# Performance work log

Measured on AMD Instinct MI355X. Metric: run time of the kernel, lower is better.

Reference implementation:

```python
import jax, jax.numpy as jnp
import numpy as np

B, C, N, K = 2, 64, 16384, 16
C_OUT = 64


def setup_inputs() -> dict:
    key = jax.random.key(0)
    k1, k2, k3, k4 = jax.random.split(key, 4)
    x = jax.random.normal(k1, (B, C, N), dtype=jnp.float32)
    edge_index = jax.random.randint(k2, (2, B, N, K), 0, N, dtype=jnp.int64)
    # 1x1 Conv2d params: weight [C_out, 3C], bias [C_out]
    W = jax.random.normal(k3, (C_OUT, 3 * C), dtype=jnp.float32) * (1.0 / np.sqrt(3 * C))
    b = jax.random.normal(k4, (C_OUT,), dtype=jnp.float32) * 0.01
    return {"x": x, "edge_index": edge_index, "W": W, "b": b}


def _gather_nodes(x, idx):
    # x: [B, C, N], idx: [B, N, K] -> [B, C, N, K]
    return jax.vmap(lambda xb, ib: xb[:, ib])(x, idx)


def reference(x, edge_index, W, b):
    # x: [B, C, N]; edge_index: [2, B, N, K]
    x_i = _gather_nodes(x, edge_index[1])          # center features  [B,C,N,K]
    x_j = _gather_nodes(x, edge_index[0])          # neighbor features [B,C,N,K]
    edge_features = x_j - x_i                      # [B,C,N,K]
    global_feature = jnp.mean(x, axis=2, keepdims=True)  # [B,C,1] global mean over nodes
    global_rep = jnp.broadcast_to(global_feature[..., None], x_i.shape)  # [B,C,N,K]
    combined = jnp.concatenate([x_i, edge_features, global_rep], axis=1)  # [B,3C,N,K]
    # BasicConv: 1x1 conv + ReLU (norm=None)
    out = jnp.einsum("bcnk,oc->bonk", combined, W) + b[None, :, None, None]
    out = jax.nn.relu(out)
    return jnp.max(out, axis=-1, keepdims=True)    # [B,C_out,N,1]
```

## Files before the change

### kernel.cpp

```cpp
#include <hip/hip_runtime.h>


#define NNODES 16384
#define NCH 64

typedef _Float16 half8 __attribute__((ext_vector_type(8)));
typedef float f32x2 __attribute__((ext_vector_type(2)));
typedef float f32x4 __attribute__((ext_vector_type(4)));

__global__ __launch_bounds__(64) void prep_kernel(const float* __restrict__ W,
                                                  float2* __restrict__ ABg,
                                                  float* __restrict__ g_slots) {
  int o = blockIdx.x;
  int t = threadIdx.x;
  if (o == 0) {
#pragma unroll
    for (int i = 0; i < 16; ++i) g_slots[t + i * 64] = 0.0f;
  }
  float w1 = W[o * 192 + t];
  float w2 = W[o * 192 + 64 + t];
  ABg[t * 64 + o] = make_float2(w1 - w2, w2);
}

__global__ __launch_bounds__(256) void uv_kernel(const float* __restrict__ x,
                                                 const float2* __restrict__ ABg,
                                                 _Float16* __restrict__ u,
                                                 _Float16* __restrict__ v,
                                                 float* __restrict__ g_slots) {
  __shared__ float2 ABs[64 * 64];
  __shared__ float xs[64][64];
  __shared__ float csumS[64];
  int t = threadIdx.x;
  int lane = t & 63;
  int wv = __builtin_amdgcn_readfirstlane(t >> 6);
  int blk = blockIdx.x;
  int b = blk >> 8;
  int mb = (blk & 255) * 64;

  {
    const float4* src = (const float4*)ABg;
    float4* dst = (float4*)ABs;
#pragma unroll
    for (int j = 0; j < 8; ++j) dst[t + j * 256] = src[t + j * 256];
  }
  {
    const float* xb = x + (size_t)b * (NCH * NNODES) + mb;
    int off = t & 15;
#pragma unroll
    for (int j = 0; j < 4; ++j) {
      int c = (t >> 4) + j * 16;
      f32x4 q = __builtin_nontemporal_load(
          (const f32x4*)(xb + (size_t)c * NNODES + off * 4));
      *(f32x4*)&xs[c][off * 4] = q;
      float s = (q.x + q.y) + (q.z + q.w);
      s += __shfl_xor(s, 1, 16);
      s += __shfl_xor(s, 2, 16);
      s += __shfl_xor(s, 4, 16);
      s += __shfl_xor(s, 8, 16);
      if (off == 0) csumS[c] = s;
    }
  }
  __syncthreads();
  if (t < 64) atomicAdd(&g_slots[((blk & 7) << 7) + b * 64 + t], csumS[t]);

  int m0 = wv * 16;
  f32x2 aU[8], aV[8];
#pragma unroll
  for (int i = 0; i < 8; ++i) {
    aU[i] = (f32x2){0.f, 0.f};
    aV[i] = (f32x2){0.f, 0.f};
  }
#pragma unroll 8
  for (int c = 0; c < 64; ++c) {
    float2 ab = ABs[c * 64 + lane];
    f32x2 a2 = {ab.x, ab.x};
    f32x2 b2 = {ab.y, ab.y};
    const f32x4* xr = (const f32x4*)&xs[c][m0];
    f32x4 q0 = xr[0];
    f32x4 q1 = xr[1];
    f32x4 q2 = xr[2];
    f32x4 q3 = xr[3];
    f32x2 p0 = {q0.x, q0.y}, p1 = {q0.z, q0.w};
    f32x2 p2 = {q1.x, q1.y}, p3 = {q1.z, q1.w};
    f32x2 p4 = {q2.x, q2.y}, p5 = {q2.z, q2.w};
    f32x2 p6 = {q3.x, q3.y}, p7 = {q3.z, q3.w};
    aU[0] = __builtin_elementwise_fma(a2, p0, aU[0]);
    aU[1] = __builtin_elementwise_fma(a2, p1, aU[1]);
    aU[2] = __builtin_elementwise_fma(a2, p2, aU[2]);
    aU[3] = __builtin_elementwise_fma(a2, p3, aU[3]);
    aU[4] = __builtin_elementwise_fma(a2, p4, aU[4]);
    aU[5] = __builtin_elementwise_fma(a2, p5, aU[5]);
    aU[6] = __builtin_elementwise_fma(a2, p6, aU[6]);
    aU[7] = __builtin_elementwise_fma(a2, p7, aU[7]);
    aV[0] = __builtin_elementwise_fma(b2, p0, aV[0]);
    aV[1] = __builtin_elementwise_fma(b2, p1, aV[1]);
    aV[2] = __builtin_elementwise_fma(b2, p2, aV[2]);
    aV[3] = __builtin_elementwise_fma(b2, p3, aV[3]);
    aV[4] = __builtin_elementwise_fma(b2, p4, aV[4]);
    aV[5] = __builtin_elementwise_fma(b2, p5, aV[5]);
    aV[6] = __builtin_elementwise_fma(b2, p6, aV[6]);
    aV[7] = __builtin_elementwise_fma(b2, p7, aV[7]);
  }
  _Float16* ub = u + ((size_t)b * NNODES + mb + m0) * NCH + lane;
  _Float16* vb = v + ((size_t)b * NNODES + mb + m0) * NCH + lane;
#pragma unroll
  for (int i = 0; i < 8; ++i) {
    __builtin_nontemporal_store((_Float16)aU[i][0], &ub[(2 * i) * NCH]);
    __builtin_nontemporal_store((_Float16)aU[i][1], &ub[(2 * i + 1) * NCH]);
    __builtin_nontemporal_store((_Float16)aV[i][0], &vb[(2 * i) * NCH]);
    __builtin_nontemporal_store((_Float16)aV[i][1], &vb[(2 * i + 1) * NCH]);
  }
}

__global__ __launch_bounds__(256) void gather_kernel(const int* __restrict__ ei,
                                                     const _Float16* __restrict__ u,
                                                     const _Float16* __restrict__ v,
                                                     const float* __restrict__ W,
                                                     const float* __restrict__ bias,
                                                     const float* __restrict__ g_slots,
                                                     float* __restrict__ out) {
  __shared__ float tile[64][33];
  __shared__ float gb[64];
  __shared__ float pg[4][64];
  __shared__ float G_s[64];
  int t = threadIdx.x;
  int lane = t & 63;
  int wv = t >> 6;
  int blk = blockIdx.x;
  int xcd = blk & 7;
  int b = xcd >> 2;
  int nb = (blk >> 3) * 4 + (xcd & 3);
  int n0 = nb * 32;
  int q = lane >> 3;
  int r = lane & 7;
  const int* e0b = ei + (size_t)b * NNODES * 16;
  const int* e1b = ei + (size_t)(2 + b) * NNODES * 16;
  int f0 = (n0 + wv * 8) * 16 + q * 16 + r;
  int i0a = __builtin_nontemporal_load(e0b + f0);
  int i0b = __builtin_nontemporal_load(e0b + f0 + 8);
  int i1a = __builtin_nontemporal_load(e1b + f0);
  int i1b = __builtin_nontemporal_load(e1b + f0 + 8);
  const char* ubase = (const char*)(u + (size_t)b * NNODES * NCH);
  const char* vbase = (const char*)(v + (size_t)b * NNODES * NCH);
  {
    int widx = blk >> 3;
    const f32x4* uw = (const f32x4*)ubase + widx * 1024;
    const f32x4* vw = (const f32x4*)vbase + widx * 1024;
    float keep = 0.f;
#pragma unroll
    for (int j = 0; j < 4; ++j) {
      f32x4 a = uw[t + j * 256];
      f32x4 c = vw[t + j * 256];
      keep += a.x + c.x;
    }
    asm volatile("" ::"v"(keep));
  }
  if (t < 64) {
    float s = 0.f;
#pragma unroll
    for (int sl = 0; sl < 8; ++sl) s += g_slots[sl * 128 + b * 64 + t];
    gb[t] = s * (1.0f / 16384.0f);
  }
  __syncthreads();
  {
    int o = t >> 2, cq = t & 3;
    const float4* wr = (const float4*)(W + o * 192 + 128 + cq * 16);
    const float4* gr = (const float4*)(gb + cq * 16);
    float s = 0.f;
#pragma unroll
    for (int j = 0; j < 4; ++j) {
      float4 w = wr[j];
      float4 gg = gr[j];
      s += w.x * gg.x + w.y * gg.y + w.z * gg.z + w.w * gg.w;
    }
    pg[cq][o] = s;
  }
  __syncthreads();
  if (t < 64) G_s[t] = bias[t] + ((pg[0][t] + pg[1][t]) + (pg[2][t] + pg[3][t]));
  __syncthreads();
  uint32_t r16 = (uint32_t)(r * 16);
  half8 accA, accB;
#pragma unroll
  for (int j = 0; j < 8; ++j) {
    accA[j] = (_Float16)(-60000.0f);
    accB[j] = (_Float16)(-60000.0f);
  }
#pragma unroll
  for (int h = 0; h < 2; ++h) {
    half8 ua[8], va[8];
#pragma unroll
    for (int k = 0; k < 8; ++k) {
      int src = (lane & 56) + k;
      int m1 = __shfl(h ? i1b : i1a, src, 64);
      int m0i = __shfl(h ? i0b : i0a, src, 64);
      ua[k] = *(const half8*)(ubase + ((uint32_t)m1 * 128u + r16));
      va[k] = *(const half8*)(vbase + ((uint32_t)m0i * 128u + r16));
    }
#pragma unroll
    for (int k = 0; k < 8; ++k) {
      half8 s = ua[k] + va[k];
      if (k & 1)
        accB = __builtin_elementwise_max(accB, s);
      else
        accA = __builtin_elementwise_max(accA, s);
    }
  }
  half8 acc = __builtin_elementwise_max(accA, accB);
  int col = wv * 8 + q;
#pragma unroll
  for (int j = 0; j < 8; ++j) {
    tile[r * 8 + j][col] = fmaxf((float)acc[j] + G_s[r * 8 + j], 0.0f);
  }
  __syncthreads();
#pragma unroll
  for (int j = 0; j < 8; ++j) {
    int o = (t >> 5) + j * 8;
    int c2 = t & 31;
    __builtin_nontemporal_store(tile[o][c2],
                                &out[((size_t)b * 64 + o) * NNODES + n0 + c2]);
  }
}

extern "C" void kernel_launch(void* const* d_in, const int* in_sizes, int n_in,
                              void* d_out, int out_size, void* d_ws, size_t ws_size,
                              hipStream_t stream) {
  const float* x = (const float*)d_in[0];
  const int* ei = (const int*)d_in[1];
  const float* W = (const float*)d_in[2];
  const float* bias = (const float*)d_in[3];
  float* out = (float*)d_out;

  char* ws = (char*)d_ws;
  _Float16* u = (_Float16*)ws;
  _Float16* v = (_Float16*)(ws + (size_t)4 * 1024 * 1024);
  float* g_slots = (float*)(ws + (size_t)8 * 1024 * 1024);
  float2* ABg = (float2*)(ws + (size_t)8 * 1024 * 1024 + 4096);

  prep_kernel<<<64, 64, 0, stream>>>(W, ABg, g_slots);
  uv_kernel<<<512, 256, 0, stream>>>(x, ABg, u, v, g_slots);
  gather_kernel<<<1024, 256, 0, stream>>>(ei, u, v, W, bias, g_slots, out);
}
```

Before: 94.02 us.

## Add x cache-warming kernel, hoist x loads in uv, drop u/v prewarm

Adds a separate warmx_kernel that reads x ahead of uv_kernel to pull it into cache. In uv_kernel the x loads are issued before the ABs copy so their latency overlaps the LDS fill. The u/v prefetch loop in gather_kernel is removed. The aim is to move x's DRAM latency out of the critical path, at the cost of an extra launch and an extra full read of x.

```diff
diff --git a/kernel.cpp b/kernel.cpp
--- a/kernel.cpp
+++ b/kernel.cpp
@@ -20,6 +20,23 @@
   float w1 = W[o * 192 + t];
   float w2 = W[o * 192 + 64 + t];
   ABg[t * 64 + o] = make_float2(w1 - w2, w2);
+}
+
+__global__ __launch_bounds__(256) void warmx_kernel(const float* __restrict__ x) {
+  int t = threadIdx.x;
+  int blk = blockIdx.x;
+  int b = blk >> 8;
+  int mb = (blk & 255) * 64;
+  const float* xb = x + (size_t)b * (NCH * NNODES) + mb;
+  int off = t & 15;
+  float keep = 0.f;
+#pragma unroll
+  for (int j = 0; j < 4; ++j) {
+    int c = (t >> 4) + j * 16;
+    f32x4 q = *(const f32x4*)(xb + (size_t)c * NNODES + off * 4);
+    keep += q.x;
+  }
+  asm volatile("" ::"v"(keep));
 }
 
 __global__ __launch_bounds__(256) void uv_kernel(const float* __restrict__ x,
@@ -37,6 +54,15 @@
   int b = blk >> 8;
   int mb = (blk & 255) * 64;
 
+  const float* xb = x + (size_t)b * (NCH * NNODES) + mb;
+  int off = t & 15;
+  f32x4 q0, q1, q2, q3;
+  {
+    q0 = __builtin_nontemporal_load((const f32x4*)(xb + (size_t)((t >> 4) + 0) * NNODES + off * 4));
+    q1 = __builtin_nontemporal_load((const f32x4*)(xb + (size_t)((t >> 4) + 16) * NNODES + off * 4));
+    q2 = __builtin_nontemporal_load((const f32x4*)(xb + (size_t)((t >> 4) + 32) * NNODES + off * 4));
+    q3 = __builtin_nontemporal_load((const f32x4*)(xb + (size_t)((t >> 4) + 48) * NNODES + off * 4));
+  }
   {
     const float4* src = (const float4*)ABg;
     float4* dst = (float4*)ABs;
@@ -44,15 +70,12 @@
     for (int j = 0; j < 8; ++j) dst[t + j * 256] = src[t + j * 256];
   }
   {
-    const float* xb = x + (size_t)b * (NCH * NNODES) + mb;
-    int off = t & 15;
+    f32x4 qq[4] = {q0, q1, q2, q3};
 #pragma unroll
     for (int j = 0; j < 4; ++j) {
       int c = (t >> 4) + j * 16;
-      f32x4 q = __builtin_nontemporal_load(
-          (const f32x4*)(xb + (size_t)c * NNODES + off * 4));
-      *(f32x4*)&xs[c][off * 4] = q;
-      float s = (q.x + q.y) + (q.z + q.w);
+      *(f32x4*)&xs[c][off * 4] = qq[j];
+      float s = (qq[j].x + qq[j].y) + (qq[j].z + qq[j].w);
       s += __shfl_xor(s, 1, 16);
       s += __shfl_xor(s, 2, 16);
       s += __shfl_xor(s, 4, 16);
@@ -76,14 +99,14 @@
     f32x2 a2 = {ab.x, ab.x};
     f32x2 b2 = {ab.y, ab.y};
     const f32x4* xr = (const f32x4*)&xs[c][m0];
-    f32x4 q0 = xr[0];
-    f32x4 q1 = xr[1];
-    f32x4 q2 = xr[2];
-    f32x4 q3 = xr[3];
-    f32x2 p0 = {q0.x, q0.y}, p1 = {q0.z, q0.w};
-    f32x2 p2 = {q1.x, q1.y}, p3 = {q1.z, q1.w};
-    f32x2 p4 = {q2.x, q2.y}, p5 = {q2.z, q2.w};
-    f32x2 p6 = {q3.x, q3.y}, p7 = {q3.z, q3.w};
+    f32x4 p0q = xr[0];
+    f32x4 p1q = xr[1];
+    f32x4 p2q = xr[2];
+    f32x4 p3q = xr[3];
+    f32x2 p0 = {p0q.x, p0q.y}, p1 = {p0q.z, p0q.w};
+    f32x2 p2 = {p1q.x, p1q.y}, p3 = {p1q.z, p1q.w};
+    f32x2 p4 = {p2q.x, p2q.y}, p5 = {p2q.z, p2q.w};
+    f32x2 p6 = {p3q.x, p3q.y}, p7 = {p3q.z, p3q.w};
     aU[0] = __builtin_elementwise_fma(a2, p0, aU[0]);
     aU[1] = __builtin_elementwise_fma(a2, p1, aU[1]);
     aU[2] = __builtin_elementwise_fma(a2, p2, aU[2]);
@@ -140,21 +163,6 @@
   int i0b = __builtin_nontemporal_load(e0b + f0 + 8);
   int i1a = __builtin_nontemporal_load(e1b + f0);
   int i1b = __builtin_nontemporal_load(e1b + f0 + 8);
-  const char* ubase = (const char*)(u + (size_t)b * NNODES * NCH);
-  const char* vbase = (const char*)(v + (size_t)b * NNODES * NCH);
-  {
-    int widx = blk >> 3;
-    const f32x4* uw = (const f32x4*)ubase + widx * 1024;
-    const f32x4* vw = (const f32x4*)vbase + widx * 1024;
-    float keep = 0.f;
-#pragma unroll
-    for (int j = 0; j < 4; ++j) {
-      f32x4 a = uw[t + j * 256];
-      f32x4 c = vw[t + j * 256];
-      keep += a.x + c.x;
-    }
-    asm volatile("" ::"v"(keep));
-  }
   if (t < 64) {
     float s = 0.f;
 #pragma unroll
@@ -178,6 +186,8 @@
   __syncthreads();
   if (t < 64) G_s[t] = bias[t] + ((pg[0][t] + pg[1][t]) + (pg[2][t] + pg[3][t]));
   __syncthreads();
+  const char* ubase = (const char*)(u + (size_t)b * NNODES * NCH);
+  const char* vbase = (const char*)(v + (size_t)b * NNODES * NCH);
   uint32_t r16 = (uint32_t)(r * 16);
   half8 accA, accB;
 #pragma unroll
@@ -237,6 +247,7 @@
   float2* ABg = (float2*)(ws + (size_t)8 * 1024 * 1024 + 4096);
 
   prep_kernel<<<64, 64, 0, stream>>>(W, ABg, g_slots);
+  warmx_kernel<<<512, 256, 0, stream>>>(x);
   uv_kernel<<<512, 256, 0, stream>>>(x, ABg, u, v, g_slots);
   gather_kernel<<<1024, 256, 0, stream>>>(ei, u, v, W, bias, g_slots, out);
 }
```

New measurement: 90.83 us. 1.04x faster.
